# Kernel tuning notes

Measured on AMD Instinct MI355X. Metric: run time of the kernel, lower is better.

The kernel has to match this reference:

```python
import jax, jax.numpy as jnp
import numpy as np

N_HOSTS = 16
N_WINDOW = 3
GAT_IN = 3
D = 16          # d_model = gat_output_feats = n_hosts
NHEAD = 2
HD = D // NHEAD # 8
FF = 64
PROTO_DIM = 8
LATENT = N_HOSTS * D * N_WINDOW  # 768
LN_EPS = 1e-5


def _positional_encoding():
    pos = np.arange(N_WINDOW, dtype=np.float32)[:, None]
    div = np.exp(np.arange(0, D, 2, dtype=np.float32) * (-np.log(10000.0) / D))
    pe = np.zeros((N_WINDOW, D), dtype=np.float32)
    pe[:, 0::2] = np.sin(pos * div)
    pe[:, 1::2] = np.cos(pos * div)
    return jnp.asarray(pe[:, None, :])  # (n_window, 1, d_model)


def setup_inputs() -> dict:
    key = jax.random.key(0)
    ks = iter(jax.random.split(key, 40))
    p = lambda *s: jax.random.normal(next(ks), s, dtype=jnp.float32) * 0.05
    inp = {
        't': jax.random.normal(next(ks), (N_WINDOW * N_HOSTS * GAT_IN,), dtype=jnp.float32),
        's': jax.random.normal(next(ks), (N_HOSTS, PROTO_DIM), dtype=jnp.float32),
        # GAT (single head, fully connected 16-node graph)
        'gat_W': p(GAT_IN, D), 'gat_a_src': p(D), 'gat_a_dst': p(D),
        # time encoder Linear(16,16)
        'te_W': p(D, D), 'te_b': p(D),
        'pe': _positional_encoding(),
        # 2 transformer encoder layers, stacked on leading axis
        'qkv_W': p(2, 3 * D, D), 'qkv_b': p(2, 3 * D),
        'out_W': p(2, D, D), 'out_b': p(2, D),
        'ln1_g': jnp.ones((2, D), jnp.float32), 'ln1_b': jnp.zeros((2, D), jnp.float32),
        'ff1_W': p(2, FF, D), 'ff1_b': p(2, FF),
        'ff2_W': p(2, D, FF), 'ff2_b': p(2, D),
        'ln2_g': jnp.ones((2, D), jnp.float32), 'ln2_b': jnp.zeros((2, D), jnp.float32),
        # decoder heads
        'an_W': p(2 * N_HOSTS, LATENT), 'an_b': p(2 * N_HOSTS),
        'pr_W': p(PROTO_DIM * N_HOSTS, LATENT), 'pr_b': p(PROTO_DIM * N_HOSTS),
    }
    return inp


def _layer_norm(x, g, b):
    m = x.mean(-1, keepdims=True)
    v = ((x - m) ** 2).mean(-1, keepdims=True)
    return (x - m) * jax.lax.rsqrt(v + LN_EPS) * g + b


def reference(t, s, gat_W, gat_a_src, gat_a_dst, te_W, te_b, pe,
              qkv_W, qkv_b, out_W, out_b, ln1_g, ln1_b,
              ff1_W, ff1_b, ff2_W, ff2_b, ln2_g, ln2_b,
              an_W, an_b, pr_W, pr_b):
    # --- GAT over fully connected 16-host graph, per window ---
    x = t.reshape(N_WINDOW, N_HOSTS, GAT_IN)
    h = x @ gat_W                                   # (w, n, D)
    e_src = h @ gat_a_src                           # (w, n)
    e_dst = h @ gat_a_dst                           # (w, n)
    e = jax.nn.leaky_relu(e_src[:, :, None] + e_dst[:, None, :], 0.2)  # (w, src, dst)
    alpha = jax.nn.softmax(e, axis=1)               # softmax over sources, per dst
    gat_out = jax.nn.elu(jnp.einsum('wsd,wsf->wdf', alpha, h))         # (w, n, D)
    # --- time encode + positional encode (dropout = identity in eval) ---
    xe = gat_out @ te_W.T + te_b + pe               # (seq=3, batch=16, D)
    # --- 2 post-norm TransformerEncoderLayers ---
    inv_sqrt_hd = 1.0 / np.sqrt(HD).astype(np.float32)
    for l in range(2):
        qkv = xe @ qkv_W[l].T + qkv_b[l]            # (s, b, 3D)
        q, k, v = jnp.split(qkv, 3, axis=-1)
        hd = lambda z: z.reshape(N_WINDOW, N_HOSTS, NHEAD, HD).transpose(1, 2, 0, 3)  # (b,h,s,hd)
        q, k, v = hd(q), hd(k), hd(v)
        att = jax.nn.softmax(jnp.einsum('bhqd,bhkd->bhqk', q, k) * inv_sqrt_hd, axis=-1)
        ctx = jnp.einsum('bhqk,bhkd->bhqd', att, v).transpose(2, 0, 1, 3).reshape(N_WINDOW, N_HOSTS, D)
        xe = _layer_norm(xe + ctx @ out_W[l].T + out_b[l], ln1_g[l], ln1_b[l])
        ff = jax.nn.relu(xe @ ff1_W[l].T + ff1_b[l]) @ ff2_W[l].T + ff2_b[l]
        xe = _layer_norm(xe + ff, ln2_g[l], ln2_b[l])
    # --- flatten to latent (batch-major, matching permute(1,0,2).reshape) ---
    latent = xe.transpose(1, 0, 2).reshape(1, LATENT)
    # nn.LeakyReLU(True): negative_slope=True==1.0, i.e. identity (faithful to source)
    anomaly = jax.nn.leaky_relu(latent @ an_W.T + an_b, 1.0).reshape(N_HOSTS, 2)
    proto = jax.nn.sigmoid(latent @ pr_W.T + pr_b).reshape(N_HOSTS, PROTO_DIM)
    return anomaly, proto
```

## Files before the change

kernel.cpp:

```cpp
#include <hip/hip_runtime.h>
#include <hip/hip_bf16.h>


#define NW 3
#define NHOST 16
#define DM 16
#define FFD 64
#define LAT 768

typedef __hip_bfloat16 bf16;
typedef __attribute__((ext_vector_type(8))) unsigned short ushort8v;
typedef __attribute__((ext_vector_type(4))) unsigned short ushort4v;

static __device__ __forceinline__ float u2f(unsigned short u) {
    return __uint_as_float(((unsigned)u) << 16);
}

static __device__ __forceinline__ float gld(const bf16* p, int i) { return __bfloat162float(p[i]); }
static __device__ __forceinline__ float gld(const float* p, int i) { return p[i]; }
static __device__ __forceinline__ void gst(bf16* p, int i, float v) { p[i] = __float2bfloat16(v); }
static __device__ __forceinline__ void gst(float* p, int i, float v) { p[i] = v; }

static __device__ __forceinline__ void ld8g(const bf16* p, float* o) {
    ushort8v v = *(const ushort8v*)p;
    #pragma unroll
    for (int u = 0; u < 8; ++u) o[u] = u2f(v[u]);
}
static __device__ __forceinline__ void ld8g(const float* p, float* o) {
    float4 a = ((const float4*)p)[0], b = ((const float4*)p)[1];
    o[0]=a.x; o[1]=a.y; o[2]=a.z; o[3]=a.w; o[4]=b.x; o[5]=b.y; o[6]=b.z; o[7]=b.w;
}
static __device__ __forceinline__ void ld4g(const bf16* p, float* o) {
    ushort4v v = *(const ushort4v*)p;
    #pragma unroll
    for (int u = 0; u < 4; ++u) o[u] = u2f(v[u]);
}
static __device__ __forceinline__ void ld4g(const float* p, float* o) {
    float4 a = *(const float4*)p;
    o[0]=a.x; o[1]=a.y; o[2]=a.z; o[3]=a.w;
}

enum {
    OFF_GATW = 0,
    OFF_ASRC = 48,
    OFF_ADST = 64,
    OFF_TEW  = 80,
    OFF_TEB  = 336,
    OFF_PE   = 352,
    OFF_QKVW = 400,
    OFF_QKVB = 1936,
    OFF_OUTW = 2032,
    OFF_OUTB = 2544,
    OFF_LN1G = 2576,
    OFF_LN1B = 2608,
    OFF_FF1W = 2640,
    OFF_FF1B = 4688,
    OFF_FF2W = 4816,
    OFF_FF2B = 6864,
    OFF_LN2G = 6896,
    OFF_LN2B = 6928,
    TOTAL_W  = 6960
};

struct __align__(16) SmemF {
    float smW[TOTAL_W];
    float hshT[768];
    float gT[768];
    float qkT[2304];
    float rT[768];
    float hT[3072];
    float latL[768];
};

template<typename T>
__device__ void fused_impl(SmemF& sm, int tid,
    const T* tin, const T* gatW, const T* asrc, const T* adst,
    const T* teW, const T* teb, const T* pe_,
    const T* qkvW, const T* qkvb, const T* outW, const T* outb,
    const T* ln1g, const T* ln1b,
    const T* ff1W, const T* ff1b, const T* ff2W, const T* ff2b,
    const T* ln2g, const T* ln2b,
    const T* anW, const T* anb, const T* prW, const T* prb,
    T* outp)
{
    float* smW = sm.smW;

    constexpr int NCHUNK = TOTAL_W / 8;
    if (tid < NCHUNK) {
        int eo = tid * 8;
        const T* p; int base;
        if      (eo < OFF_ASRC) { p = gatW;  base = OFF_GATW; }
        else if (eo < OFF_ADST) { p = asrc;  base = OFF_ASRC; }
        else if (eo < OFF_TEW)  { p = adst;  base = OFF_ADST; }
        else if (eo < OFF_TEB)  { p = teW;   base = OFF_TEW; }
        else if (eo < OFF_PE)   { p = teb;   base = OFF_TEB; }
        else if (eo < OFF_QKVW) { p = pe_;   base = OFF_PE; }
        else if (eo < OFF_QKVB) { p = qkvW;  base = OFF_QKVW; }
        else if (eo < OFF_OUTW) { p = qkvb;  base = OFF_QKVB; }
        else if (eo < OFF_OUTB) { p = outW;  base = OFF_OUTW; }
        else if (eo < OFF_LN1G) { p = outb;  base = OFF_OUTB; }
        else if (eo < OFF_LN1B) { p = ln1g;  base = OFF_LN1G; }
        else if (eo < OFF_FF1W) { p = ln1b;  base = OFF_LN1B; }
        else if (eo < OFF_FF1B) { p = ff1W;  base = OFF_FF1W; }
        else if (eo < OFF_FF2W) { p = ff1b;  base = OFF_FF1B; }
        else if (eo < OFF_FF2B) { p = ff2W;  base = OFF_FF2W; }
        else if (eo < OFF_LN2G) { p = ff2b;  base = OFF_FF2B; }
        else if (eo < OFF_LN2B) { p = ln2g;  base = OFF_LN2G; }
        else                    { p = ln2b;  base = OFF_LN2B; }
        float v[8];
        ld8g(p + (eo - base), v);
        *(float4*)&smW[eo]     = float4{v[0], v[1], v[2], v[3]};
        *(float4*)&smW[eo + 4] = float4{v[4], v[5], v[6], v[7]};
    }

    const int lane = tid & 63;
    const int wid  = tid >> 6;
    const int tok  = lane < 48 ? lane : 47;
    const int w = tok >> 4, n = tok & 15;

    float t0 = gld(tin, tok * 3 + 0), t1 = gld(tin, tok * 3 + 1), t2 = gld(tin, tok * 3 + 2);
    __syncthreads();

    float h[16];
    #pragma unroll
    for (int f = 0; f < 16; ++f) {
        float acc = 0.f;
        acc += t0 * smW[OFF_GATW + f];
        acc += t1 * smW[OFF_GATW + 16 + f];
        acc += t2 * smW[OFF_GATW + 32 + f];
        h[f] = acc;
    }
    float es = 0.f, ed = 0.f;
    #pragma unroll
    for (int f = 0; f < 16; ++f) es += h[f] * smW[OFF_ASRC + f];
    #pragma unroll
    for (int f = 0; f < 16; ++f) ed += h[f] * smW[OFF_ADST + f];

    if (wid == 0 && lane < 48) {
        #pragma unroll
        for (int f = 0; f < 16; ++f) sm.hshT[f * 48 + tok] = h[f];
    }
    __syncthreads();

    float e[16];
    float mx = -1e30f;
    #pragma unroll
    for (int s = 0; s < 16; ++s) {
        float xv = __shfl(es, (tok & 48) + s) + ed;
        xv = xv > 0.f ? xv : 0.2f * xv;
        e[s] = xv;
        mx = fmaxf(mx, xv);
    }
    float sum = 0.f;
    #pragma unroll
    for (int s = 0; s < 16; ++s) { e[s] = __expf(e[s] - mx); sum += e[s]; }
    float inv = 1.f / sum;

    {
        const float* hp = &sm.hshT[wid * 48 + (w << 4)];
        float go = 0.f;
        #pragma unroll
        for (int s = 0; s < 16; ++s) { float as = e[s] * inv; go += as * hp[s]; }
        go = go > 0.f ? go : __expf(go) - 1.f;
        if (lane < 48) sm.gT[wid * 48 + tok] = go;
    }
    __syncthreads();

    {
        float acc = smW[OFF_TEB + wid] + smW[OFF_PE + (w << 4) + wid];
        #pragma unroll
        for (int g = 0; g < 16; ++g) acc += sm.gT[g * 48 + tok] * smW[OFF_TEW + wid * 16 + g];
        if (lane < 48) sm.rT[wid * 48 + tok] = acc;
    }
    __syncthreads();

    float x[16];
    #pragma unroll
    for (int f = 0; f < 16; ++f) x[f] = sm.rT[f * 48 + tok];

    for (int l = 0; l < 2; ++l) {
        const int qW = OFF_QKVW + l * 768, qb = OFF_QKVB + l * 48;
        {
            const int j0 = wid * 3;
            float qo[3];
            #pragma unroll
            for (int jj = 0; jj < 3; ++jj) {
                int j = j0 + jj;
                float acc = smW[qb + j];
                #pragma unroll
                for (int f = 0; f < 16; ++f) acc += x[f] * smW[qW + j * 16 + f];
                qo[jj] = acc;
            }
            if (lane < 48) {
                #pragma unroll
                for (int jj = 0; jj < 3; ++jj) sm.qkT[(j0 + jj) * 48 + tok] = qo[jj];
            }
        }
        __syncthreads();

        if (wid < 4) {
            const int hb = (wid >> 1) * 8;
            const float inv_sqrt_hd = 0.35355339059327373f;
            float qv[8];
            #pragma unroll
            for (int d = 0; d < 8; ++d) qv[d] = sm.qkT[(hb + d) * 48 + tok];
            float sc[3];
            #pragma unroll
            for (int ks = 0; ks < 3; ++ks) {
                int src = (tok & 15) + (ks << 4);
                float acc = 0.f;
                #pragma unroll
                for (int d = 0; d < 8; ++d) acc += qv[d] * sm.qkT[(16 + hb + d) * 48 + src];
                sc[ks] = acc * inv_sqrt_hd;
            }
            float m2 = fmaxf(sc[0], fmaxf(sc[1], sc[2]));
            float s0 = __expf(sc[0] - m2), s1 = __expf(sc[1] - m2), s2 = __expf(sc[2] - m2);
            float iv = 1.f / (s0 + s1 + s2);
            s0 *= iv; s1 *= iv; s2 *= iv;
            const int src0 = (tok & 15);
            #pragma unroll
            for (int dd = 0; dd < 4; ++dd) {
                int d = wid * 4 + dd;
                float c = s0 * sm.qkT[(32 + d) * 48 + src0];
                c += s1 * sm.qkT[(32 + d) * 48 + src0 + 16];
                c += s2 * sm.qkT[(32 + d) * 48 + src0 + 32];
                if (lane < 48) sm.gT[d * 48 + tok] = c;
            }
        }
        __syncthreads();

        const int oW = OFF_OUTW + l * 256, ob = OFF_OUTB + l * 16;
        {
            float acc = smW[ob + wid] + x[wid];
            #pragma unroll
            for (int g = 0; g < 16; ++g) acc += sm.gT[g * 48 + tok] * smW[oW + wid * 16 + g];
            if (lane < 48) sm.rT[wid * 48 + tok] = acc;
        }
        __syncthreads();

        {
            float r[16];
            #pragma unroll
            for (int f = 0; f < 16; ++f) r[f] = sm.rT[f * 48 + tok];
            float m = 0.f;
            #pragma unroll
            for (int f = 0; f < 16; ++f) m += r[f];
            m *= (1.f / 16.f);
            float v = 0.f;
            #pragma unroll
            for (int f = 0; f < 16; ++f) { float d0 = r[f] - m; v += d0 * d0; }
            v *= (1.f / 16.f);
            float rr = rsqrtf(v + 1e-5f);
            #pragma unroll
            for (int f = 0; f < 16; ++f)
                x[f] = (r[f] - m) * rr * smW[OFF_LN1G + l * 16 + f] + smW[OFF_LN1B + l * 16 + f];
        }

        const int f1W = OFF_FF1W + l * 1024, f1b = OFF_FF1B + l * 64;
        {
            #pragma unroll
            for (int jj = 0; jj < 4; ++jj) {
                int j = wid * 4 + jj;
                float hj = smW[f1b + j];
                #pragma unroll
                for (int f = 0; f < 16; ++f) hj += x[f] * smW[f1W + j * 16 + f];
                hj = fmaxf(hj, 0.f);
                if (lane < 48) sm.hT[j * 48 + tok] = hj;
            }
        }
        __syncthreads();

        const int f2W = OFF_FF2W + l * 1024;
        {
            float acc = 0.f;
            #pragma unroll
            for (int j = 0; j < 64; ++j) acc += sm.hT[j * 48 + tok] * smW[f2W + wid * 64 + j];
            if (lane < 48) sm.rT[wid * 48 + tok] = acc;
        }
        __syncthreads();

        {
            const int f2b = OFF_FF2B + l * 16;
            float fa[16];
            #pragma unroll
            for (int f = 0; f < 16; ++f) fa[f] = x[f] + (sm.rT[f * 48 + tok] + smW[f2b + f]);
            float m = 0.f;
            #pragma unroll
            for (int f = 0; f < 16; ++f) m += fa[f];
            m *= (1.f / 16.f);
            float v = 0.f;
            #pragma unroll
            for (int f = 0; f < 16; ++f) { float d0 = fa[f] - m; v += d0 * d0; }
            v *= (1.f / 16.f);
            float rr = rsqrtf(v + 1e-5f);
            #pragma unroll
            for (int f = 0; f < 16; ++f)
                x[f] = (fa[f] - m) * rr * smW[OFF_LN2G + l * 16 + f] + smW[OFF_LN2B + l * 16 + f];
        }
    }

    if (wid == 0 && lane < 48) {
        float* lp = &sm.latL[n * 48 + (w << 4)];
        #pragma unroll
        for (int q = 0; q < 4; ++q)
            *(float4*)&lp[q * 4] = float4{x[q*4], x[q*4+1], x[q*4+2], x[q*4+3]};
    }
    __syncthreads();

    float4 la = ((const float4*)sm.latL)[2 * lane];
    float4 lb = ((const float4*)sm.latL)[2 * lane + 1];
    float4 lc = ((const float4*)(sm.latL + 512))[lane];

    #pragma unroll 2
    for (int rr = 0; rr < 10; ++rr) {
        int o = wid * 10 + rr;
        const T* Wr = (o < 32) ? (anW + o * LAT) : (prW + (o - 32) * LAT);
        float wv8[8], wv4[4];
        ld8g(Wr + lane * 8, wv8);
        ld4g(Wr + 512 + lane * 4, wv4);
        float acc = wv8[0]*la.x + wv8[1]*la.y + wv8[2]*la.z + wv8[3]*la.w
                  + wv8[4]*lb.x + wv8[5]*lb.y + wv8[6]*lb.z + wv8[7]*lb.w
                  + wv4[0]*lc.x + wv4[1]*lc.y + wv4[2]*lc.z + wv4[3]*lc.w;
        #pragma unroll
        for (int m = 1; m < 64; m <<= 1) acc += __shfl_xor(acc, m);
        if (lane == 0) {
            if (o < 32) {
                gst(outp, o, acc + gld(anb, o));
            } else {
                float z = acc + gld(prb, o - 32);
                gst(outp, o, 1.f / (1.f + __expf(-z)));
            }
        }
    }
}

__global__ void __launch_bounds__(1024) txf_fused(
    const void* t, const void* gat_W, const void* a_src, const void* a_dst,
    const void* te_W, const void* te_b, const void* pe,
    const void* qkv_W, const void* qkv_b, const void* out_W, const void* out_b,
    const void* ln1_g, const void* ln1_b,
    const void* ff1_W, const void* ff1_b, const void* ff2_W, const void* ff2_b,
    const void* ln2_g, const void* ln2_b,
    const void* an_W, const void* an_b, const void* pr_W, const void* pr_b,
    void* outp)
{
    __shared__ SmemF sm;
    const int tid = threadIdx.x;
    unsigned w0 = *(const unsigned*)ln1_g;
    if (w0 == 0x3F803F80u) {
        fused_impl<bf16>(sm, tid,
            (const bf16*)t, (const bf16*)gat_W, (const bf16*)a_src, (const bf16*)a_dst,
            (const bf16*)te_W, (const bf16*)te_b, (const bf16*)pe,
            (const bf16*)qkv_W, (const bf16*)qkv_b, (const bf16*)out_W, (const bf16*)out_b,
            (const bf16*)ln1_g, (const bf16*)ln1_b,
            (const bf16*)ff1_W, (const bf16*)ff1_b, (const bf16*)ff2_W, (const bf16*)ff2_b,
            (const bf16*)ln2_g, (const bf16*)ln2_b,
            (const bf16*)an_W, (const bf16*)an_b, (const bf16*)pr_W, (const bf16*)pr_b,
            (bf16*)outp);
    } else {
        fused_impl<float>(sm, tid,
            (const float*)t, (const float*)gat_W, (const float*)a_src, (const float*)a_dst,
            (const float*)te_W, (const float*)te_b, (const float*)pe,
            (const float*)qkv_W, (const float*)qkv_b, (const float*)out_W, (const float*)out_b,
            (const float*)ln1_g, (const float*)ln1_b,
            (const float*)ff1_W, (const float*)ff1_b, (const float*)ff2_W, (const float*)ff2_b,
            (const float*)ln2_g, (const float*)ln2_b,
            (const float*)an_W, (const float*)an_b, (const float*)pr_W, (const float*)pr_b,
            (float*)outp);
    }
}

extern "C" void kernel_launch(void* const* d_in, const int* in_sizes, int n_in,
                              void* d_out, int out_size, void* d_ws, size_t ws_size,
                              hipStream_t stream) {
    (void)d_ws; (void)ws_size;

    txf_fused<<<1, 1024, 0, stream>>>(
        d_in[0],
        d_in[2], d_in[3], d_in[4],
        d_in[5], d_in[6], d_in[7],
        d_in[8], d_in[9], d_in[10], d_in[11],
        d_in[12], d_in[13],
        d_in[14], d_in[15], d_in[16], d_in[17],
        d_in[18], d_in[19],
        d_in[20], d_in[21], d_in[22], d_in[23],
        d_out);
}
```

Baseline: 120.6 us.

## Halve block size, switch smem to token-major padded layout, prefetch decoder weights

Drops the block from 1024 to 512 threads, so each wavefront computes more output features per stage. Shared-memory intermediates change from feature-major to token-major rows with padded strides, which allows vectorized float4 loads and stores. At kernel start every thread touches one element per cache line of the anomaly and prototype decoder weights, warming caches so the later GEMV does not stall on DRAM. The decoder bias loads are hoisted and broadcast via shuffle; the trade-off is fewer waves and more serial work per wave.

After: 126.3 us. +4.8%, slower.

```diff
diff --git a/kernel.cpp b/kernel.cpp
--- a/kernel.cpp
+++ b/kernel.cpp
@@ -8,6 +8,10 @@
 #define FFD 64
 #define LAT 768
 
+#define SG 20
+#define SQ 52
+#define SH 68
+
 typedef __hip_bfloat16 bf16;
 typedef __attribute__((ext_vector_type(8))) unsigned short ushort8v;
 typedef __attribute__((ext_vector_type(4))) unsigned short ushort4v;
@@ -38,6 +42,15 @@
 static __device__ __forceinline__ void ld4g(const float* p, float* o) {
     float4 a = *(const float4*)p;
     o[0]=a.x; o[1]=a.y; o[2]=a.z; o[3]=a.w;
+}
+
+static __device__ __forceinline__ void ld16(const float* p, float* o) {
+    float4 a = ((const float4*)p)[0], b = ((const float4*)p)[1],
+           c = ((const float4*)p)[2], d = ((const float4*)p)[3];
+    o[0]=a.x; o[1]=a.y; o[2]=a.z; o[3]=a.w;
+    o[4]=b.x; o[5]=b.y; o[6]=b.z; o[7]=b.w;
+    o[8]=c.x; o[9]=c.y; o[10]=c.z; o[11]=c.w;
+    o[12]=d.x; o[13]=d.y; o[14]=d.z; o[15]=d.w;
 }
 
 enum {
@@ -64,12 +77,12 @@
 
 struct __align__(16) SmemF {
     float smW[TOTAL_W];
-    float hshT[768];
-    float gT[768];
-    float qkT[2304];
-    float rT[768];
-    float hT[3072];
-    float latL[768];
+    float hsh[768];
+    float gT[48 * SG];
+    float rT[48 * SG];
+    float rT2[48 * SG];
+    float qkT[48 * SQ];
+    float hT[48 * SH];
 };
 
 template<typename T>
@@ -84,10 +97,21 @@
     T* outp)
 {
     float* smW = sm.smW;
+    const int lane = tid & 63;
+    const int wid  = tid >> 6;
+    const int tok  = lane < 48 ? lane : 47;
+    const int w = tok >> 4;
+
+    float sink = 0.f;
+    {
+        constexpr int STR = 64 / (int)sizeof(T);
+        for (int i = tid; i * STR < 32 * LAT; i += 512)  sink += gld(anW, i * STR);
+        for (int i = tid; i * STR < 128 * LAT; i += 512) sink += gld(prW, i * STR);
+    }
 
     constexpr int NCHUNK = TOTAL_W / 8;
-    if (tid < NCHUNK) {
-        int eo = tid * 8;
+    for (int g = tid; g < NCHUNK; g += 512) {
+        int eo = g * 8;
         const T* p; int base;
         if      (eo < OFF_ASRC) { p = gatW;  base = OFF_GATW; }
         else if (eo < OFF_ADST) { p = asrc;  base = OFF_ASRC; }
@@ -113,32 +137,34 @@
         *(float4*)&smW[eo + 4] = float4{v[4], v[5], v[6], v[7]};
     }
 
-    const int lane = tid & 63;
-    const int wid  = tid >> 6;
-    const int tok  = lane < 48 ? lane : 47;
-    const int w = tok >> 4, n = tok & 15;
-
     float t0 = gld(tin, tok * 3 + 0), t1 = gld(tin, tok * 3 + 1), t2 = gld(tin, tok * 3 + 2);
     __syncthreads();
 
     float h[16];
-    #pragma unroll
-    for (int f = 0; f < 16; ++f) {
-        float acc = 0.f;
-        acc += t0 * smW[OFF_GATW + f];
-        acc += t1 * smW[OFF_GATW + 16 + f];
-        acc += t2 * smW[OFF_GATW + 32 + f];
-        h[f] = acc;
+    {
+        float g0[16], g1[16], g2[16];
+        ld16(&smW[OFF_GATW], g0); ld16(&smW[OFF_GATW + 16], g1); ld16(&smW[OFF_GATW + 32], g2);
+        #pragma unroll
+        for (int f = 0; f < 16; ++f) {
+            float acc = 0.f;
+            acc += t0 * g0[f];
+            acc += t1 * g1[f];
+            acc += t2 * g2[f];
+            h[f] = acc;
+        }
     }
     float es = 0.f, ed = 0.f;
-    #pragma unroll
-    for (int f = 0; f < 16; ++f) es += h[f] * smW[OFF_ASRC + f];
-    #pragma unroll
-    for (int f = 0; f < 16; ++f) ed += h[f] * smW[OFF_ADST + f];
-
+    {
+        float av[16], dv[16];
+        ld16(&smW[OFF_ASRC], av); ld16(&smW[OFF_ADST], dv);
+        #pragma unroll
+        for (int f = 0; f < 16; ++f) es += h[f] * av[f];
+        #pragma unroll
+        for (int f = 0; f < 16; ++f) ed += h[f] * dv[f];
+    }
     if (wid == 0 && lane < 48) {
         #pragma unroll
-        for (int f = 0; f < 16; ++f) sm.hshT[f * 48 + tok] = h[f];
+        for (int f = 0; f < 16; ++f) sm.hsh[f * 48 + tok] = h[f];
     }
     __syncthreads();
 
@@ -157,43 +183,61 @@
     float inv = 1.f / sum;
 
     {
-        const float* hp = &sm.hshT[wid * 48 + (w << 4)];
-        float go = 0.f;
-        #pragma unroll
-        for (int s = 0; s < 16; ++s) { float as = e[s] * inv; go += as * hp[s]; }
-        go = go > 0.f ? go : __expf(go) - 1.f;
-        if (lane < 48) sm.gT[wid * 48 + tok] = go;
+        float go2[2];
+        #pragma unroll
+        for (int ff = 0; ff < 2; ++ff) {
+            int f = wid * 2 + ff;
+            float hp[16];
+            ld16(&sm.hsh[f * 48 + (w << 4)], hp);
+            float acc = 0.f;
+            #pragma unroll
+            for (int s = 0; s < 16; ++s) { float as = e[s] * inv; acc += as * hp[s]; }
+            go2[ff] = acc > 0.f ? acc : __expf(acc) - 1.f;
+        }
+        if (lane < 48) *(float2*)&sm.gT[tok * SG + wid * 2] = float2{go2[0], go2[1]};
     }
     __syncthreads();
 
     {
-        float acc = smW[OFF_TEB + wid] + smW[OFF_PE + (w << 4) + wid];
-        #pragma unroll
-        for (int g = 0; g < 16; ++g) acc += sm.gT[g * 48 + tok] * smW[OFF_TEW + wid * 16 + g];
-        if (lane < 48) sm.rT[wid * 48 + tok] = acc;
+        float gv[16];
+        ld16(&sm.gT[tok * SG], gv);
+        float o2[2];
+        #pragma unroll
+        for (int ff = 0; ff < 2; ++ff) {
+            int f = wid * 2 + ff;
+            float wr[16];
+            ld16(&smW[OFF_TEW + f * 16], wr);
+            float acc = smW[OFF_TEB + f] + smW[OFF_PE + (w << 4) + f];
+            #pragma unroll
+            for (int g2 = 0; g2 < 16; ++g2) acc += gv[g2] * wr[g2];
+            o2[ff] = acc;
+        }
+        if (lane < 48) *(float2*)&sm.rT[tok * SG + wid * 2] = float2{o2[0], o2[1]};
     }
     __syncthreads();
 
     float x[16];
-    #pragma unroll
-    for (int f = 0; f < 16; ++f) x[f] = sm.rT[f * 48 + tok];
+    ld16(&sm.rT[tok * SG], x);
 
     for (int l = 0; l < 2; ++l) {
         const int qW = OFF_QKVW + l * 768, qb = OFF_QKVB + l * 48;
         {
-            const int j0 = wid * 3;
-            float qo[3];
-            #pragma unroll
-            for (int jj = 0; jj < 3; ++jj) {
-                int j = j0 + jj;
+            float qo[6];
+            #pragma unroll
+            for (int jj = 0; jj < 6; ++jj) {
+                int j = wid * 6 + jj;
+                float wr[16];
+                ld16(&smW[qW + j * 16], wr);
                 float acc = smW[qb + j];
                 #pragma unroll
-                for (int f = 0; f < 16; ++f) acc += x[f] * smW[qW + j * 16 + f];
+                for (int f = 0; f < 16; ++f) acc += x[f] * wr[f];
                 qo[jj] = acc;
             }
             if (lane < 48) {
-                #pragma unroll
-                for (int jj = 0; jj < 3; ++jj) sm.qkT[(j0 + jj) * 48 + tok] = qo[jj];
+                float* qp = &sm.qkT[tok * SQ + wid * 6];
+                *(float2*)&qp[0] = float2{qo[0], qo[1]};
+                *(float2*)&qp[2] = float2{qo[2], qo[3]};
+                *(float2*)&qp[4] = float2{qo[4], qo[5]};
             }
         }
         __syncthreads();
@@ -202,46 +246,64 @@
             const int hb = (wid >> 1) * 8;
             const float inv_sqrt_hd = 0.35355339059327373f;
             float qv[8];
-            #pragma unroll
-            for (int d = 0; d < 8; ++d) qv[d] = sm.qkT[(hb + d) * 48 + tok];
+            {
+                float4 a = *(const float4*)&sm.qkT[tok * SQ + hb];
+                float4 b = *(const float4*)&sm.qkT[tok * SQ + hb + 4];
+                qv[0]=a.x; qv[1]=a.y; qv[2]=a.z; qv[3]=a.w;
+                qv[4]=b.x; qv[5]=b.y; qv[6]=b.z; qv[7]=b.w;
+            }
             float sc[3];
             #pragma unroll
             for (int ks = 0; ks < 3; ++ks) {
                 int src = (tok & 15) + (ks << 4);
+                float4 k0 = *(const float4*)&sm.qkT[src * SQ + 16 + hb];
+                float4 k1 = *(const float4*)&sm.qkT[src * SQ + 16 + hb + 4];
                 float acc = 0.f;
-                #pragma unroll
-                for (int d = 0; d < 8; ++d) acc += qv[d] * sm.qkT[(16 + hb + d) * 48 + src];
+                acc += qv[0]*k0.x; acc += qv[1]*k0.y; acc += qv[2]*k0.z; acc += qv[3]*k0.w;
+                acc += qv[4]*k1.x; acc += qv[5]*k1.y; acc += qv[6]*k1.z; acc += qv[7]*k1.w;
                 sc[ks] = acc * inv_sqrt_hd;
             }
             float m2 = fmaxf(sc[0], fmaxf(sc[1], sc[2]));
             float s0 = __expf(sc[0] - m2), s1 = __expf(sc[1] - m2), s2 = __expf(sc[2] - m2);
             float iv = 1.f / (s0 + s1 + s2);
             s0 *= iv; s1 *= iv; s2 *= iv;
-            const int src0 = (tok & 15);
-            #pragma unroll
-            for (int dd = 0; dd < 4; ++dd) {
-                int d = wid * 4 + dd;
-                float c = s0 * sm.qkT[(32 + d) * 48 + src0];
-                c += s1 * sm.qkT[(32 + d) * 48 + src0 + 16];
-                c += s2 * sm.qkT[(32 + d) * 48 + src0 + 32];
-                if (lane < 48) sm.gT[d * 48 + tok] = c;
-            }
+            float c0, c1, c2, c3;
+            {
+                int src = (tok & 15);
+                float4 v0 = *(const float4*)&sm.qkT[src * SQ + 32 + wid * 4];
+                float4 v1 = *(const float4*)&sm.qkT[(src + 16) * SQ + 32 + wid * 4];
+                float4 v2 = *(const float4*)&sm.qkT[(src + 32) * SQ + 32 + wid * 4];
+                c0 = s0 * v0.x + s1 * v1.x + s2 * v2.x;
+                c1 = s0 * v0.y + s1 * v1.y + s2 * v2.y;
+                c2 = s0 * v0.z + s1 * v1.z + s2 * v2.z;
+                c3 = s0 * v0.w + s1 * v1.w + s2 * v2.w;
+            }
+            if (lane < 48) *(float4*)&sm.gT[tok * SG + wid * 4] = float4{c0, c1, c2, c3};
         }
         __syncthreads();
 
         const int oW = OFF_OUTW + l * 256, ob = OFF_OUTB + l * 16;
-        {
-            float acc = smW[ob + wid] + x[wid];
-            #pragma unroll
-            for (int g = 0; g < 16; ++g) acc += sm.gT[g * 48 + tok] * smW[oW + wid * 16 + g];
-            if (lane < 48) sm.rT[wid * 48 + tok] = acc;
+        if (wid < 4) {
+            float ctx[16];
+            ld16(&sm.gT[tok * SG], ctx);
+            float rv[4];
+            #pragma unroll
+            for (int ff = 0; ff < 4; ++ff) {
+                int f = wid * 4 + ff;
+                float wr[16];
+                ld16(&smW[oW + f * 16], wr);
+                float acc = smW[ob + f] + x[f];
+                #pragma unroll
+                for (int g2 = 0; g2 < 16; ++g2) acc += ctx[g2] * wr[g2];
+                rv[ff] = acc;
+            }
+            if (lane < 48) *(float4*)&sm.rT[tok * SG + wid * 4] = float4{rv[0], rv[1], rv[2], rv[3]};
         }
         __syncthreads();
 
         {
             float r[16];
-            #pragma unroll
-            for (int f = 0; f < 16; ++f) r[f] = sm.rT[f * 48 + tok];
+            ld16(&sm.rT[tok * SG], r);
             float m = 0.f;
             #pragma unroll
             for (int f = 0; f < 16; ++f) m += r[f];
@@ -251,39 +313,60 @@
             for (int f = 0; f < 16; ++f) { float d0 = r[f] - m; v += d0 * d0; }
             v *= (1.f / 16.f);
             float rr = rsqrtf(v + 1e-5f);
-            #pragma unroll
-            for (int f = 0; f < 16; ++f)
-                x[f] = (r[f] - m) * rr * smW[OFF_LN1G + l * 16 + f] + smW[OFF_LN1B + l * 16 + f];
+            float gp[16], bp[16];
+            ld16(&smW[OFF_LN1G + l * 16], gp); ld16(&smW[OFF_LN1B + l * 16], bp);
+            #pragma unroll
+            for (int f = 0; f < 16; ++f) x[f] = (r[f] - m) * rr * gp[f] + bp[f];
         }
 
         const int f1W = OFF_FF1W + l * 1024, f1b = OFF_FF1B + l * 64;
         {
-            #pragma unroll
-            for (int jj = 0; jj < 4; ++jj) {
-                int j = wid * 4 + jj;
-                float hj = smW[f1b + j];
+            float hv[8];
+            #pragma unroll
+            for (int jj = 0; jj < 8; ++jj) {
+                int j = wid * 8 + jj;
+                float wr[16];
+                ld16(&smW[f1W + j * 16], wr);
+                float acc = smW[f1b + j];
                 #pragma unroll
-                for (int f = 0; f < 16; ++f) hj += x[f] * smW[f1W + j * 16 + f];
-                hj = fmaxf(hj, 0.f);
-                if (lane < 48) sm.hT[j * 48 + tok] = hj;
+                for (int f = 0; f < 16; ++f) acc += x[f] * wr[f];
+                hv[jj] = fmaxf(acc, 0.f);
+            }
+            if (lane < 48) {
+                *(float4*)&sm.hT[tok * SH + wid * 8]     = float4{hv[0], hv[1], hv[2], hv[3]};
+                *(float4*)&sm.hT[tok * SH + wid * 8 + 4] = float4{hv[4], hv[5], hv[6], hv[7]};
             }
         }
         __syncthreads();
 
         const int f2W = OFF_FF2W + l * 1024;
-        {
-            float acc = 0.f;
-            #pragma unroll
-            for (int j = 0; j < 64; ++j) acc += sm.hT[j * 48 + tok] * smW[f2W + wid * 64 + j];
-            if (lane < 48) sm.rT[wid * 48 + tok] = acc;
+        if (wid < 4) {
+            float a0 = 0.f, a1 = 0.f, a2 = 0.f, a3 = 0.f;
+            #pragma unroll
+            for (int c = 0; c < 16; ++c) {
+                float4 hv = *(const float4*)&sm.hT[tok * SH + c * 4];
+                float4 w0 = *(const float4*)&smW[f2W + (wid * 4 + 0) * 64 + c * 4];
+                float4 w1 = *(const float4*)&smW[f2W + (wid * 4 + 1) * 64 + c * 4];
+                float4 w2 = *(const float4*)&smW[f2W + (wid * 4 + 2) * 64 + c * 4];
+                float4 w3 = *(const float4*)&smW[f2W + (wid * 4 + 3) * 64 + c * 4];
+                a0 += hv.x*w0.x; a0 += hv.y*w0.y; a0 += hv.z*w0.z; a0 += hv.w*w0.w;
+                a1 += hv.x*w1.x; a1 += hv.y*w1.y; a1 += hv.z*w1.z; a1 += hv.w*w1.w;
+                a2 += hv.x*w2.x; a2 += hv.y*w2.y; a2 += hv.z*w2.z; a2 += hv.w*w2.w;
+                a3 += hv.x*w3.x; a3 += hv.y*w3.y; a3 += hv.z*w3.z; a3 += hv.w*w3.w;
+            }
+            if (lane < 48) *(float4*)&sm.rT2[tok * SG + wid * 4] = float4{a0, a1, a2, a3};
         }
         __syncthreads();
 
         {
             const int f2b = OFF_FF2B + l * 16;
+            float r2[16];
+            ld16(&sm.rT2[tok * SG], r2);
+            float fb[16];
+            ld16(&smW[f2b], fb);
             float fa[16];
             #pragma unroll
-            for (int f = 0; f < 16; ++f) fa[f] = x[f] + (sm.rT[f * 48 + tok] + smW[f2b + f]);
+            for (int f = 0; f < 16; ++f) fa[f] = x[f] + (r2[f] + fb[f]);
             float m = 0.f;
             #pragma unroll
             for (int f = 0; f < 16; ++f) m += fa[f];
@@ -293,48 +376,69 @@
             for (int f = 0; f < 16; ++f) { float d0 = fa[f] - m; v += d0 * d0; }
             v *= (1.f / 16.f);
             float rr = rsqrtf(v + 1e-5f);
-            #pragma unroll
-            for (int f = 0; f < 16; ++f)
-                x[f] = (fa[f] - m) * rr * smW[OFF_LN2G + l * 16 + f] + smW[OFF_LN2B + l * 16 + f];
+            float gp[16], bp[16];
+            ld16(&smW[OFF_LN2G + l * 16], gp); ld16(&smW[OFF_LN2B + l * 16], bp);
+            #pragma unroll
+            for (int f = 0; f < 16; ++f) x[f] = (fa[f] - m) * rr * gp[f] + bp[f];
         }
     }
 
     if (wid == 0 && lane < 48) {
-        float* lp = &sm.latL[n * 48 + (w << 4)];
-        #pragma unroll
-        for (int q = 0; q < 4; ++q)
-            *(float4*)&lp[q * 4] = float4{x[q*4], x[q*4+1], x[q*4+2], x[q*4+3]};
+        float* lp = &sm.rT[tok * SG];
+        *(float4*)&lp[0]  = float4{x[0],  x[1],  x[2],  x[3]};
+        *(float4*)&lp[4]  = float4{x[4],  x[5],  x[6],  x[7]};
+        *(float4*)&lp[8]  = float4{x[8],  x[9],  x[10], x[11]};
+        *(float4*)&lp[12] = float4{x[12], x[13], x[14], x[15]};
     }
     __syncthreads();
 
-    float4 la = ((const float4*)sm.latL)[2 * lane];
-    float4 lb = ((const float4*)sm.latL)[2 * lane + 1];
-    float4 lc = ((const float4*)(sm.latL + 512))[lane];
-
-    #pragma unroll 2
-    for (int rr = 0; rr < 10; ++rr) {
-        int o = wid * 10 + rr;
+    float la[8], lc[4];
+    {
+        int i0 = lane * 8;
+        int n0 = i0 / 48, r0 = i0 % 48, w0 = r0 >> 4, f0 = r0 & 15;
+        const float* L0 = &sm.rT[(w0 * 16 + n0) * SG + f0];
+        float4 a = *(const float4*)&L0[0];
+        float4 b = *(const float4*)&L0[4];
+        la[0]=a.x; la[1]=a.y; la[2]=a.z; la[3]=a.w;
+        la[4]=b.x; la[5]=b.y; la[6]=b.z; la[7]=b.w;
+        int i1 = 512 + lane * 4;
+        int n1 = i1 / 48, r1 = i1 % 48, w1 = r1 >> 4, f1 = r1 & 15;
+        float4 c = *(const float4*)&sm.rT[(w1 * 16 + n1) * SG + f1];
+        lc[0]=c.x; lc[1]=c.y; lc[2]=c.z; lc[3]=c.w;
+    }
+    float bv = 0.f;
+    if (lane < 20) {
+        int o = wid * 20 + lane;
+        bv = (o < 32) ? gld(anb, o) : gld(prb, o - 32);
+    }
+
+    #pragma unroll 4
+    for (int rr = 0; rr < 20; ++rr) {
+        int o = wid * 20 + rr;
         const T* Wr = (o < 32) ? (anW + o * LAT) : (prW + (o - 32) * LAT);
         float wv8[8], wv4[4];
         ld8g(Wr + lane * 8, wv8);
         ld4g(Wr + 512 + lane * 4, wv4);
-        float acc = wv8[0]*la.x + wv8[1]*la.y + wv8[2]*la.z + wv8[3]*la.w
-                  + wv8[4]*lb.x + wv8[5]*lb.y + wv8[6]*lb.z + wv8[7]*lb.w
-                  + wv4[0]*lc.x + wv4[1]*lc.y + wv4[2]*lc.z + wv4[3]*lc.w;
+        float acc = wv8[0]*la[0] + wv8[1]*la[1] + wv8[2]*la[2] + wv8[3]*la[3]
+                  + wv8[4]*la[4] + wv8[5]*la[5] + wv8[6]*la[6] + wv8[7]*la[7]
+                  + wv4[0]*lc[0] + wv4[1]*lc[1] + wv4[2]*lc[2] + wv4[3]*lc[3];
         #pragma unroll
         for (int m = 1; m < 64; m <<= 1) acc += __shfl_xor(acc, m);
+        float bb = __shfl(bv, rr);
         if (lane == 0) {
             if (o < 32) {
-                gst(outp, o, acc + gld(anb, o));
+                gst(outp, o, acc + bb);
             } else {
-                float z = acc + gld(prb, o - 32);
+                float z = acc + bb;
                 gst(outp, o, 1.f / (1.f + __expf(-z)));
             }
         }
     }
-}
-
-__global__ void __launch_bounds__(1024) txf_fused(
+
+    asm volatile("" :: "v"(sink));
+}
+
+__global__ void __launch_bounds__(512) txf_fused(
     const void* t, const void* gat_W, const void* a_src, const void* a_dst,
     const void* te_W, const void* te_b, const void* pe,
     const void* qkv_W, const void* qkv_b, const void* out_W, const void* out_b,
@@ -375,7 +479,7 @@
                               hipStream_t stream) {
     (void)d_ws; (void)ws_size;
 
-    txf_fused<<<1, 1024, 0, stream>>>(
+    txf_fused<<<1, 512, 0, stream>>>(
         d_in[0],
         d_in[2], d_in[3], d_in[4],
         d_in[5], d_in[6], d_in[7],
```
